# Kernel optimization log

Hardware: AMD Instinct MI355X
Metric: run time of the kernel (lower is better)

Reference implementation:

```python
import jax, jax.numpy as jnp
import numpy as np

D_MODEL = 2048
D_KV = 512
D_Q = 1536
N_HEADS = 16
HEAD_DIM = 128
ROPE_BASE = 10000.0


def apply_rope(x, past_len=0):
    # x: [B, H, S, D]; interleaved-pair rotation (pairs (2i, 2i+1))
    B, H, S, D = x.shape
    half = D // 2
    pos = (jnp.arange(S) + past_len).astype(jnp.float32)
    inv_freq = 1.0 / (ROPE_BASE ** (jnp.arange(half, dtype=jnp.float32) * 2.0 / D))
    ang = pos[:, None] * inv_freq[None, :]          # [S, half]
    cos, sin = jnp.cos(ang), jnp.sin(ang)
    x1 = x[..., 0::2]
    x2 = x[..., 1::2]
    r1 = x1 * cos - x2 * sin
    r2 = x1 * sin + x2 * cos
    return jnp.stack([r1, r2], axis=-1).reshape(x.shape)


def setup_inputs() -> dict:
    key = jax.random.key(0)
    ks = jax.random.split(key, 16)
    s = 0.02
    inp = {
        "h": jax.random.normal(ks[0], (2, 2048, D_MODEL), dtype=jnp.float32),
        # weights stored [in, out] (y = x @ W + b)
        "W_DKV": jax.random.normal(ks[1], (D_MODEL, D_KV)) * s,
        "b_DKV": jnp.zeros((D_KV,)),
        "W_UK": jax.random.normal(ks[2], (D_KV, N_HEADS * HEAD_DIM)) * s,
        "b_UK": jnp.zeros((N_HEADS * HEAD_DIM,)),
        "W_UV": jax.random.normal(ks[3], (D_KV, N_HEADS * HEAD_DIM)) * s,
        "b_UV": jnp.zeros((N_HEADS * HEAD_DIM,)),
        "W_DQ": jax.random.normal(ks[4], (D_MODEL, D_Q)) * s,
        "b_DQ": jnp.zeros((D_Q,)),
        "W_UQ": jax.random.normal(ks[5], (D_Q, N_HEADS * HEAD_DIM)) * s,
        "b_UQ": jnp.zeros((N_HEADS * HEAD_DIM,)),
        "W_KR": jax.random.normal(ks[6], (D_MODEL, D_MODEL)) * s,
        "b_KR": jnp.zeros((D_MODEL,)),
        "W_O": jax.random.normal(ks[7], (D_MODEL, D_MODEL)) * s,
        "b_O": jnp.zeros((D_MODEL,)),
    }
    return inp


def reference(h, W_DKV, b_DKV, W_UK, b_UK, W_UV, b_UV, W_DQ, b_DQ,
              W_UQ, b_UQ, W_KR, b_KR, W_O, b_O):
    B, S, _ = h.shape

    def split_heads(x):  # [B,S,H*D] -> [B,H,S,D]
        return x.reshape(B, S, N_HEADS, HEAD_DIM).transpose(0, 2, 1, 3)

    # latent KV path (prefill: no cache)
    c_KV = h @ W_DKV + b_DKV                     # [B,S,d_kv] latent cache
    k_C = split_heads(c_KV @ W_UK + b_UK)        # [B,H,S,Dh]
    v_C = split_heads(c_KV @ W_UV + b_UV)        # [B,H,S,Dh]

    # decoupled RoPE K path
    kr_cache = h @ W_KR + b_KR                   # [B,S,d_model]
    k_R = apply_rope(split_heads(kr_cache))      # [B,H,S,Dh]
    k = jnp.concatenate([k_C, k_R], axis=-1)     # [B,H,S,2*Dh]

    # latent Q path
    c_Q = h @ W_DQ + b_DQ
    q_C = split_heads(c_Q @ W_UQ + b_UQ)
    q_R = apply_rope(q_C, past_len=0)
    q = jnp.concatenate([q_C, q_R], axis=-1)     # [B,H,S,2*Dh]

    # causal attention
    scale = 1.0 / jnp.sqrt(jnp.float32(q.shape[-1]))
    scores = jnp.einsum("bhqd,bhkd->bhqk", q, k) * scale
    causal = jnp.tril(jnp.ones((S, S), dtype=bool))
    scores = jnp.where(causal, scores, jnp.finfo(scores.dtype).min)
    attn = jax.nn.softmax(scores, axis=-1)
    ctx = jnp.einsum("bhqk,bhkd->bhqd", attn, v_C)
    ctx = ctx.transpose(0, 2, 1, 3).reshape(B, S, N_HEADS * HEAD_DIM)
    out = ctx @ W_O + b_O
    return (out, c_KV, kr_cache)
```

## Files before the change

### kernel.cpp

```cpp
#include <hip/hip_runtime.h>
#include <cstdint>
#include <cstddef>

typedef __bf16 bf16;
typedef __bf16 bf16x8 __attribute__((ext_vector_type(8)));
typedef float  f32x4  __attribute__((ext_vector_type(4)));

#define INVF_C 0.20762050593046014f

__device__ __forceinline__ void async_copy16(const void* g, void* l)
{
    auto gp = (__attribute__((address_space(1))) const void*)(reinterpret_cast<uintptr_t>(g));
    auto lp = (__attribute__((address_space(3))) void*)(uint32_t)(reinterpret_cast<uintptr_t>(l));
    __builtin_amdgcn_global_load_lds(gp, lp, 16, 0, 0);
}

__global__ void cast_to_bf16(const float* __restrict__ in, bf16* __restrict__ out, int n)
{
    const int i = (blockIdx.x * 256 + threadIdx.x) * 4;
    if (i < n) {
        const float4 v = *(const float4*)(in + i);
        out[i]     = (bf16)v.x;
        out[i + 1] = (bf16)v.y;
        out[i + 2] = (bf16)v.z;
        out[i + 3] = (bf16)v.w;
    }
}

__global__ void transpose_cast(const float* __restrict__ in, bf16* __restrict__ out,
                               int R, int Ccols)
{
    __shared__ float tile[32][33];
    const int c0 = blockIdx.x * 32;
    const int r0 = blockIdx.y * 32;
    const int tx = threadIdx.x, ty = threadIdx.y;
    for (int i = ty; i < 32; i += 8)
        tile[i][tx] = in[(size_t)(r0 + i) * Ccols + c0 + tx];
    __syncthreads();
    for (int i = ty; i < 32; i += 8)
        out[(size_t)(c0 + i) * R + r0 + tx] = (bf16)tile[tx][i];
}

__device__ __forceinline__ void gemm_core(const bf16* __restrict__ A,
                                          const bf16* __restrict__ Bt,
                                          int K, int m0, int n0,
                                          bf16* As, bf16* Bs,
                                          f32x4 (&acc)[4][4])
{
    const int tid  = threadIdx.x;
    const int wave = tid >> 6;
    const int lane = tid & 63;
    const int quad = lane >> 4;
    const int l15  = lane & 15;
    const int wm   = (wave >> 1) * 64;
    const int wn   = (wave & 1) * 64;

    const int srow = lane >> 3;
    const int scol = (lane & 7) * 8;
    const bf16* Ab = A  + (size_t)(m0 + wave * 32 + srow) * K + scol;
    const bf16* Bb = Bt + (size_t)(n0 + wave * 32 + srow) * K + scol;
    bf16* AsW = &As[(wave * 32) * 64];
    bf16* BsW = &Bs[(wave * 32) * 64];

    for (int k0 = 0; k0 < K; k0 += 64) {
        __syncthreads();
#pragma unroll
        for (int i = 0; i < 4; ++i) {
            async_copy16(Ab + (size_t)(i * 8) * K + k0, AsW + i * 8 * 64);
            async_copy16(Bb + (size_t)(i * 8) * K + k0, BsW + i * 8 * 64);
        }
        __syncthreads();
#pragma unroll
        for (int ks = 0; ks < 2; ++ks) {
            bf16x8 af[4], bfr[4];
#pragma unroll
            for (int i = 0; i < 4; ++i)
                af[i] = *(const bf16x8*)&As[(wm + i * 16 + l15) * 64 + ks * 32 + quad * 8];
#pragma unroll
            for (int j = 0; j < 4; ++j)
                bfr[j] = *(const bf16x8*)&Bs[(wn + j * 16 + l15) * 64 + ks * 32 + quad * 8];
#pragma unroll
            for (int i = 0; i < 4; ++i)
#pragma unroll
                for (int j = 0; j < 4; ++j)
                    acc[i][j] = __builtin_amdgcn_mfma_f32_16x16x32_bf16(af[i], bfr[j], acc[i][j], 0, 0, 0);
        }
    }
}

__global__ __launch_bounds__(256, 2)
void gemm_bt(const bf16* __restrict__ A, const bf16* __restrict__ Bt,
             const float* __restrict__ bias, float* __restrict__ C,
             bf16* __restrict__ Cb, int M, int N, int K)
{
    __shared__ bf16 As[128 * 64];
    __shared__ bf16 Bs[128 * 64];
    const int m0 = blockIdx.y * 128;
    const int n0 = blockIdx.x * 128;
    f32x4 acc[4][4] = {};
    gemm_core(A, Bt, K, m0, n0, As, Bs, acc);

    const int tid  = threadIdx.x;
    const int wave = tid >> 6;
    const int lane = tid & 63;
    const int quad = lane >> 4;
    const int l15  = lane & 15;
    const int wm   = (wave >> 1) * 64;
    const int wn   = (wave & 1) * 64;

#pragma unroll
    for (int j = 0; j < 4; ++j) {
        const int col = n0 + wn + j * 16 + l15;
        const float bv = bias[col];
#pragma unroll
        for (int i = 0; i < 4; ++i) {
            const int row = m0 + wm + i * 16 + quad * 4;
#pragma unroll
            for (int r = 0; r < 4; ++r) {
                const float v = acc[i][j][r] + bv;
                if (C)  C [(size_t)(row + r) * N + col] = v;
                if (Cb) Cb[(size_t)(row + r) * N + col] = (bf16)v;
            }
        }
    }
}

__global__ __launch_bounds__(256, 2)
void gemm_batch1(const bf16* __restrict__ A, const bf16* __restrict__ WtAll,
                 const float* __restrict__ bDKV, const float* __restrict__ bKR,
                 const float* __restrict__ bDQ,
                 float* __restrict__ cKV_f, bf16* __restrict__ cKVb,
                 float* __restrict__ krc_f, bf16* __restrict__ cQ)
{
    __shared__ bf16 As[128 * 64];
    __shared__ bf16 Bs[128 * 64];
    const int m0 = blockIdx.y * 128;
    const int n0 = blockIdx.x * 128;
    f32x4 acc[4][4] = {};
    gemm_core(A, WtAll, 2048, m0, n0, As, Bs, acc);

    const int tid  = threadIdx.x;
    const int wave = tid >> 6;
    const int lane = tid & 63;
    const int quad = lane >> 4;
    const int l15  = lane & 15;
    const int wm   = (wave >> 1) * 64;
    const int wn   = (wave & 1) * 64;

    if (n0 < 512) {
#pragma unroll
        for (int j = 0; j < 4; ++j) {
            const int col = n0 + wn + j * 16 + l15;
            const float bv = bDKV[col];
#pragma unroll
            for (int i = 0; i < 4; ++i) {
                const int row = m0 + wm + i * 16 + quad * 4;
#pragma unroll
                for (int r = 0; r < 4; ++r) {
                    const float v = acc[i][j][r] + bv;
                    cKV_f[(size_t)(row + r) * 512 + col] = v;
                    cKVb [(size_t)(row + r) * 512 + col] = (bf16)v;
                }
            }
        }
    } else if (n0 < 2560) {
#pragma unroll
        for (int j = 0; j < 4; ++j) {
            const int col = n0 + wn + j * 16 + l15;
            const int cl  = col - 512;
            const float bv = bKR[cl];
#pragma unroll
            for (int i = 0; i < 4; ++i) {
                const int row = m0 + wm + i * 16 + quad * 4;
#pragma unroll
                for (int r = 0; r < 4; ++r)
                    krc_f[(size_t)(row + r) * 2048 + cl] = acc[i][j][r] + bv;
            }
        }
    } else {
#pragma unroll
        for (int j = 0; j < 4; ++j) {
            const int col = n0 + wn + j * 16 + l15;
            const int cl  = col - 2560;
            const float bv = bDQ[cl];
#pragma unroll
            for (int i = 0; i < 4; ++i) {
                const int row = m0 + wm + i * 16 + quad * 4;
#pragma unroll
                for (int r = 0; r < 4; ++r)
                    cQ[(size_t)(row + r) * 1536 + cl] = (bf16)(acc[i][j][r] + bv);
            }
        }
    }
}

__global__ __launch_bounds__(256, 2)
void gemm_batch45(const bf16* __restrict__ A, const bf16* __restrict__ Wt45,
                  const float* __restrict__ bUK, const float* __restrict__ bUV,
                  bf16* __restrict__ kC, bf16* __restrict__ vC)
{
    __shared__ bf16 As[128 * 64];
    __shared__ bf16 Bs[128 * 64];
    const int m0 = blockIdx.y * 128;
    const int n0 = blockIdx.x * 128;
    f32x4 acc[4][4] = {};
    gemm_core(A, Wt45, 512, m0, n0, As, Bs, acc);

    const int tid  = threadIdx.x;
    const int wave = tid >> 6;
    const int lane = tid & 63;
    const int quad = lane >> 4;
    const int l15  = lane & 15;
    const int wm   = (wave >> 1) * 64;
    const int wn   = (wave & 1) * 64;

    const bool isK = (n0 < 2048);
    bf16* outp = isK ? kC : vC;
    const float* bp = isK ? bUK : bUV;
    const int base = isK ? 0 : 2048;
#pragma unroll
    for (int j = 0; j < 4; ++j) {
        const int col = n0 + wn + j * 16 + l15;
        const int cl  = col - base;
        const float bv = bp[cl];
#pragma unroll
        for (int i = 0; i < 4; ++i) {
            const int row = m0 + wm + i * 16 + quad * 4;
#pragma unroll
            for (int r = 0; r < 4; ++r)
                outp[(size_t)(row + r) * 2048 + cl] = (bf16)(acc[i][j][r] + bv);
        }
    }
}

__global__ __launch_bounds__(256, 2)
void gemm_q_rope(const bf16* __restrict__ A, const bf16* __restrict__ Bt,
                 const float* __restrict__ bias,
                 bf16* __restrict__ qC, bf16* __restrict__ qR)
{
    __shared__ bf16 As[128 * 64];
    __shared__ bf16 Bs[128 * 64];
    const int m0 = blockIdx.y * 128;
    const int n0 = blockIdx.x * 128;
    f32x4 acc[4][4] = {};
    gemm_core(A, Bt, 1536, m0, n0, As, Bs, acc);

    const int tid  = threadIdx.x;
    const int wave = tid >> 6;
    const int lane = tid & 63;
    const int quad = lane >> 4;
    const int l15  = lane & 15;
    const int wm   = (wave >> 1) * 64;
    const int wn   = (wave & 1) * 64;
    const int odd  = l15 & 1;

#pragma unroll
    for (int j = 0; j < 4; ++j) {
        const int col = n0 + wn + j * 16 + l15;
        const float bv = bias[col];
        const float freq = exp2f(-(float)((col & 127) >> 1) * INVF_C);
#pragma unroll
        for (int i = 0; i < 4; ++i) {
            const int rowb = m0 + wm + i * 16 + quad * 4;
#pragma unroll
            for (int r = 0; r < 4; ++r) {
                const int row = rowb + r;
                const float v = acc[i][j][r] + bv;
                qC[(size_t)row * 2048 + col] = (bf16)v;
                const float vp = __shfl_xor(v, 1, 64);
                const float x1 = odd ? vp : v;
                const float x2 = odd ? v  : vp;
                const float ang = (float)(row & 2047) * freq;
                float sn, cs;
                __sincosf(ang, &sn, &cs);
                qR[(size_t)row * 2048 + col] =
                    (bf16)(odd ? (x1 * sn + x2 * cs) : (x1 * cs - x2 * sn));
            }
        }
    }
}

__global__ void transpose_v(const bf16* __restrict__ vC, bf16* __restrict__ vT)
{
    __shared__ bf16 tile[32][33];
    const int bh = blockIdx.z, b = bh >> 4, h = bh & 15;
    const int s0 = blockIdx.x * 32, d0 = blockIdx.y * 32;
    const int tx = threadIdx.x, ty = threadIdx.y;
    for (int i = ty; i < 32; i += 8)
        tile[i][tx] = vC[((size_t)(b * 2048 + s0 + i)) * 2048 + h * 128 + d0 + tx];
    __syncthreads();
    for (int i = ty; i < 32; i += 8)
        vT[((size_t)(bh * 128 + d0 + i)) * 2048 + s0 + tx] = tile[tx][i];
}

__global__ void rope_heads_f(const float* __restrict__ in, bf16* __restrict__ out)
{
    const int idx = blockIdx.x * 256 + threadIdx.x;
    const int j = idx & 63;
    const int h = (idx >> 6) & 15;
    const int s = (idx >> 10) & 2047;
    const int b = idx >> 21;
    const size_t src = ((size_t)(b * 2048 + s)) * 2048 + h * 128 + 2 * j;
    const float x1 = in[src], x2 = in[src + 1];
    const float ang = (float)s * exp2f(-(float)j * INVF_C);
    float sn, cs;
    __sincosf(ang, &sn, &cs);
    out[src]     = (bf16)(x1 * cs - x2 * sn);
    out[src + 1] = (bf16)(x1 * sn + x2 * cs);
}

__global__ __launch_bounds__(512, 2)
void mla_attn(const bf16* __restrict__ qCp, const bf16* __restrict__ qRp,
              const bf16* __restrict__ kCp, const bf16* __restrict__ kRp,
              const bf16* __restrict__ Vt, bf16* __restrict__ ctx)
{
    __shared__ bf16 Ks[64 * 264];
    __shared__ bf16 Vs[128 * 72];
    __shared__ bf16 Ps[128 * 72];
    const int bh   = blockIdx.x;
    const int b    = bh >> 4, hh = bh & 15;
    const int yq   = blockIdx.y;
    const int qt   = (yq < 8) ? (2 * yq) : (31 - 2 * yq);
    const int q0   = qt * 128;
    const int tid  = threadIdx.x;
    const int wave = tid >> 6;
    const int lane = tid & 63;
    const int quad = lane >> 4;
    const int l15  = lane & 15;
    const int wq   = q0 + wave * 16;

    bf16x8 qf[8];
    {
        const size_t qoff = ((size_t)(b * 2048 + wq + l15)) * 2048
                          + hh * 128 + quad * 8;
#pragma unroll
        for (int ks = 0; ks < 4; ++ks) {
            qf[ks]     = *(const bf16x8*)(qCp + qoff + ks * 32);
            qf[4 + ks] = *(const bf16x8*)(qRp + qoff + ks * 32);
        }
    }

    float mstate[4], lstate[4];
    f32x4 o[8];
#pragma unroll
    for (int r = 0; r < 4; ++r) { mstate[r] = -1e30f; lstate[r] = 0.0f; }
#pragma unroll
    for (int dt = 0; dt < 8; ++dt) { f32x4 z = {0.f, 0.f, 0.f, 0.f}; o[dt] = z; }

    const int krow = tid >> 4, kcol = (tid & 15) * 8;
    const int vsr  = tid >> 3, vsc  = (tid & 7) * 8;

    const int ntiles = 2 * qt + 2;
    for (int t = 0; t < ntiles; ++t) {
        const int kk0 = t * 64;
        __syncthreads();
#pragma unroll
        for (int it = 0; it < 2; ++it) {
            const int row = it * 32 + krow;
            const size_t g = ((size_t)(b * 2048 + kk0 + row)) * 2048 + hh * 128 + kcol;
            *(bf16x8*)&Ks[row * 264 + kcol]       = *(const bf16x8*)(kCp + g);
            *(bf16x8*)&Ks[row * 264 + 128 + kcol] = *(const bf16x8*)(kRp + g);
        }
#pragma unroll
        for (int it = 0; it < 2; ++it) {
            const int d = it * 64 + vsr;
            *(bf16x8*)&Vs[d * 72 + vsc] =
                *(const bf16x8*)(Vt + ((size_t)(bh * 128 + d)) * 2048 + kk0 + vsc);
        }
        __syncthreads();

        if (kk0 <= wq + 15) {
            f32x4 sc[4] = {};
#pragma unroll
            for (int ks = 0; ks < 8; ++ks)
#pragma unroll
                for (int j = 0; j < 4; ++j) {
                    bf16x8 kf = *(const bf16x8*)&Ks[(j * 16 + l15) * 264 + ks * 32 + quad * 8];
                    sc[j] = __builtin_amdgcn_mfma_f32_16x16x32_bf16(qf[ks], kf, sc[j], 0, 0, 0);
                }

            const bool diag = (kk0 + 63 > wq);
            float rowmax[4] = {-1e30f, -1e30f, -1e30f, -1e30f};
#pragma unroll
            for (int j = 0; j < 4; ++j) {
                const int kkcol = kk0 + j * 16 + l15;
#pragma unroll
                for (int r = 0; r < 4; ++r) {
                    float s = sc[j][r] * 0.0625f;
                    if (diag && (kkcol > wq + quad * 4 + r)) s = -1e30f;
                    sc[j][r] = s;
                    rowmax[r] = fmaxf(rowmax[r], s);
                }
            }
#pragma unroll
            for (int r = 0; r < 4; ++r) {
                float v = rowmax[r];
                v = fmaxf(v, __shfl_xor(v, 1, 64));
                v = fmaxf(v, __shfl_xor(v, 2, 64));
                v = fmaxf(v, __shfl_xor(v, 4, 64));
                v = fmaxf(v, __shfl_xor(v, 8, 64));
                rowmax[r] = v;
            }
            float alpha[4];
#pragma unroll
            for (int r = 0; r < 4; ++r) {
                const float mnew = fmaxf(mstate[r], rowmax[r]);
                alpha[r] = __expf(mstate[r] - mnew);
                mstate[r] = mnew;
            }
            float rowsum[4] = {0.f, 0.f, 0.f, 0.f};
#pragma unroll
            for (int j = 0; j < 4; ++j)
#pragma unroll
                for (int r = 0; r < 4; ++r) {
                    const float p = __expf(sc[j][r] - mstate[r]);
                    sc[j][r] = p;
                    rowsum[r] += p;
                }
#pragma unroll
            for (int r = 0; r < 4; ++r) {
                float v = rowsum[r];
                v += __shfl_xor(v, 1, 64);
                v += __shfl_xor(v, 2, 64);
                v += __shfl_xor(v, 4, 64);
                v += __shfl_xor(v, 8, 64);
                lstate[r] = lstate[r] * alpha[r] + v;
            }
#pragma unroll
            for (int j = 0; j < 4; ++j)
#pragma unroll
                for (int r = 0; r < 4; ++r)
                    Ps[(wave * 16 + quad * 4 + r) * 72 + j * 16 + l15] = (bf16)sc[j][r];
#pragma unroll
            for (int dt = 0; dt < 8; ++dt)
#pragma unroll
                for (int r = 0; r < 4; ++r)
                    o[dt][r] *= alpha[r];
#pragma unroll
            for (int ks2 = 0; ks2 < 2; ++ks2) {
                bf16x8 pf = *(const bf16x8*)&Ps[(wave * 16 + l15) * 72 + ks2 * 32 + quad * 8];
#pragma unroll
                for (int dt = 0; dt < 8; ++dt) {
                    bf16x8 vf = *(const bf16x8*)&Vs[(dt * 16 + l15) * 72 + ks2 * 32 + quad * 8];
                    o[dt] = __builtin_amdgcn_mfma_f32_16x16x32_bf16(pf, vf, o[dt], 0, 0, 0);
                }
            }
        }
    }

    float inv_l[4];
#pragma unroll
    for (int r = 0; r < 4; ++r) inv_l[r] = 1.0f / lstate[r];
#pragma unroll
    for (int dt = 0; dt < 8; ++dt) {
        const int d = dt * 16 + l15;
#pragma unroll
        for (int r = 0; r < 4; ++r) {
            const int q = wq + quad * 4 + r;
            ctx[((size_t)(b * 2048 + q)) * 2048 + hh * 128 + d] = (bf16)(o[dt][r] * inv_l[r]);
        }
    }
}

extern "C" void kernel_launch(void* const* d_in, const int* in_sizes, int n_in,
                              void* d_out, int out_size, void* d_ws, size_t ws_size,
                              hipStream_t stream)
{
    const float* h     = (const float*)d_in[0];
    const float* W_DKV = (const float*)d_in[1];
    const float* b_DKV = (const float*)d_in[2];
    const float* W_UK  = (const float*)d_in[3];
    const float* b_UK  = (const float*)d_in[4];
    const float* W_UV  = (const float*)d_in[5];
    const float* b_UV  = (const float*)d_in[6];
    const float* W_DQ  = (const float*)d_in[7];
    const float* b_DQ  = (const float*)d_in[8];
    const float* W_UQ  = (const float*)d_in[9];
    const float* b_UQ  = (const float*)d_in[10];
    const float* W_KR  = (const float*)d_in[11];
    const float* b_KR  = (const float*)d_in[12];
    const float* W_O   = (const float*)d_in[13];
    const float* b_O   = (const float*)d_in[14];

    float* out   = (float*)d_out;
    float* cKV_f = out + (size_t)8388608;
    float* krc_f = out + (size_t)10485760;

    bf16* qC = (bf16*)d_out;
    bf16* qR = (bf16*)d_out + 8388608;

    bf16* ws    = (bf16*)d_ws;
    bf16* hb    = ws + 0;
    bf16* cKVb  = ws + 8388608;
    bf16* cQ    = ws + 10485760;
    bf16* WtAll = ws + 16777216;
    bf16* kC    = ws + 25165824;
    bf16* vC    = ws + 33554432;
    bf16* kR    = hb;
    bf16* vT    = WtAll;
    bf16* ctx   = vC;

    dim3 tb(32, 8);

    cast_to_bf16<<<8192, 256, 0, stream>>>(h, hb, 8388608);

    transpose_cast<<<dim3(16, 64), tb, 0, stream>>>(W_DKV, WtAll,                 2048, 512);
    transpose_cast<<<dim3(64, 64), tb, 0, stream>>>(W_KR,  WtAll + 1048576,       2048, 2048);
    transpose_cast<<<dim3(48, 64), tb, 0, stream>>>(W_DQ,  WtAll + 5242880,       2048, 1536);

    gemm_batch1<<<dim3(32, 32), 256, 0, stream>>>(hb, WtAll, b_DKV, b_KR, b_DQ,
                                                  cKV_f, cKVb, krc_f, cQ);
    rope_heads_f<<<16384, 256, 0, stream>>>(krc_f, kR);

    transpose_cast<<<dim3(64, 16), tb, 0, stream>>>(W_UK, WtAll,           512, 2048);
    transpose_cast<<<dim3(64, 16), tb, 0, stream>>>(W_UV, WtAll + 1048576, 512, 2048);
    gemm_batch45<<<dim3(32, 32), 256, 0, stream>>>(cKVb, WtAll, b_UK, b_UV, kC, vC);

    transpose_cast<<<dim3(64, 48), tb, 0, stream>>>(W_UQ, WtAll, 1536, 2048);
    gemm_q_rope<<<dim3(16, 32), 256, 0, stream>>>(cQ, WtAll, b_UQ, qC, qR);

    transpose_v<<<dim3(64, 4, 32), tb, 0, stream>>>(vC, vT);

    mla_attn<<<dim3(32, 16), 512, 0, stream>>>(qC, qR, kC, kR, vT, ctx);

    transpose_cast<<<dim3(64, 64), tb, 0, stream>>>(W_O, WtAll, 2048, 2048);
    gemm_bt<<<dim3(16, 32), 256, 0, stream>>>(ctx, WtAll, b_O, out, nullptr, 4096, 2048, 2048);
}
```

Measured before the change: 541.1 us.

## Widen transpose tiles, swizzle GEMM blocks per XCD, lazy softmax rescale

The weight transpose-cast kernel now works on 64x64 tiles with float4 loads and paired bf16 stores, to cut memory-transaction overhead. All GEMM kernels remap block indices so consecutive tiles land on the same XCD, aiming for better L2 reuse. In the attention kernel, the online-softmax rescale of the output and running sum now happens only when some row max grows by more than a threshold. MFMA sections are bracketed with s_setprio raises. The lazy rescale gives up exact running-max tracking, which changes numerics slightly and relies on exp values staying bounded by the threshold.

New measurement: 591.3 us. 9.3% more time.

```diff
diff --git a/kernel.cpp b/kernel.cpp
--- a/kernel.cpp
+++ b/kernel.cpp
@@ -3,6 +3,7 @@
 #include <cstddef>
 
 typedef __bf16 bf16;
+typedef __bf16 bf16x2 __attribute__((ext_vector_type(2)));
 typedef __bf16 bf16x8 __attribute__((ext_vector_type(8)));
 typedef float  f32x4  __attribute__((ext_vector_type(4)));
 
@@ -27,18 +28,43 @@
     }
 }
 
-__global__ void transpose_cast(const float* __restrict__ in, bf16* __restrict__ out,
-                               int R, int Ccols)
-{
-    __shared__ float tile[32][33];
-    const int c0 = blockIdx.x * 32;
-    const int r0 = blockIdx.y * 32;
-    const int tx = threadIdx.x, ty = threadIdx.y;
-    for (int i = ty; i < 32; i += 8)
-        tile[i][tx] = in[(size_t)(r0 + i) * Ccols + c0 + tx];
+__global__ __launch_bounds__(256)
+void transpose_cast(const float* __restrict__ in, bf16* __restrict__ out,
+                    int R, int Ccols)
+{
+    __shared__ float tile[64][65];
+    const int c0 = blockIdx.x * 64;
+    const int r0 = blockIdx.y * 64;
+    const int tid = threadIdx.x;
+    const int lr = tid >> 4;
+    const int lc = (tid & 15) * 4;
+#pragma unroll
+    for (int i = 0; i < 4; ++i) {
+        const int row = i * 16 + lr;
+        const float4 v = *(const float4*)(in + (size_t)(r0 + row) * Ccols + c0 + lc);
+        tile[row][lc]     = v.x;
+        tile[row][lc + 1] = v.y;
+        tile[row][lc + 2] = v.z;
+        tile[row][lc + 3] = v.w;
+    }
     __syncthreads();
-    for (int i = ty; i < 32; i += 8)
-        out[(size_t)(c0 + i) * R + r0 + tx] = (bf16)tile[tx][i];
+    const int rr  = (tid & 31) * 2;
+    const int cc0 = tid >> 5;
+#pragma unroll
+    for (int i = 0; i < 8; ++i) {
+        const int cc = i * 8 + cc0;
+        bf16x2 p = { (bf16)tile[rr][cc], (bf16)tile[rr + 1][cc] };
+        *(bf16x2*)(out + (size_t)(c0 + cc) * R + r0 + rr) = p;
+    }
+}
+
+__device__ __forceinline__ void xcd_tile(int& m0, int& n0)
+{
+    const int bid = blockIdx.y * gridDim.x + blockIdx.x;
+    const int cpx = (gridDim.x * gridDim.y) >> 3;
+    const int swz = (bid & 7) * cpx + (bid >> 3);
+    m0 = (swz / gridDim.x) * 128;
+    n0 = (swz % gridDim.x) * 128;
 }
 
 __device__ __forceinline__ void gemm_core(const bf16* __restrict__ A,
@@ -95,8 +121,8 @@
 {
     __shared__ bf16 As[128 * 64];
     __shared__ bf16 Bs[128 * 64];
-    const int m0 = blockIdx.y * 128;
-    const int n0 = blockIdx.x * 128;
+    int m0, n0;
+    xcd_tile(m0, n0);
     f32x4 acc[4][4] = {};
     gemm_core(A, Bt, K, m0, n0, As, Bs, acc);
 
@@ -134,8 +160,8 @@
 {
     __shared__ bf16 As[128 * 64];
     __shared__ bf16 Bs[128 * 64];
-    const int m0 = blockIdx.y * 128;
-    const int n0 = blockIdx.x * 128;
+    int m0, n0;
+    xcd_tile(m0, n0);
     f32x4 acc[4][4] = {};
     gemm_core(A, WtAll, 2048, m0, n0, As, Bs, acc);
 
@@ -201,8 +227,8 @@
 {
     __shared__ bf16 As[128 * 64];
     __shared__ bf16 Bs[128 * 64];
-    const int m0 = blockIdx.y * 128;
-    const int n0 = blockIdx.x * 128;
+    int m0, n0;
+    xcd_tile(m0, n0);
     f32x4 acc[4][4] = {};
     gemm_core(A, Wt45, 512, m0, n0, As, Bs, acc);
 
@@ -240,8 +266,8 @@
 {
     __shared__ bf16 As[128 * 64];
     __shared__ bf16 Bs[128 * 64];
-    const int m0 = blockIdx.y * 128;
-    const int n0 = blockIdx.x * 128;
+    int m0, n0;
+    xcd_tile(m0, n0);
     f32x4 acc[4][4] = {};
     gemm_core(A, Bt, 1536, m0, n0, As, Bs, acc);
 
@@ -371,6 +397,7 @@
 
         if (kk0 <= wq + 15) {
             f32x4 sc[4] = {};
+            __builtin_amdgcn_s_setprio(1);
 #pragma unroll
             for (int ks = 0; ks < 8; ++ks)
 #pragma unroll
@@ -378,6 +405,7 @@
                     bf16x8 kf = *(const bf16x8*)&Ks[(j * 16 + l15) * 264 + ks * 32 + quad * 8];
                     sc[j] = __builtin_amdgcn_mfma_f32_16x16x32_bf16(qf[ks], kf, sc[j], 0, 0, 0);
                 }
+            __builtin_amdgcn_s_setprio(0);
 
             const bool diag = (kk0 + 63 > wq);
             float rowmax[4] = {-1e30f, -1e30f, -1e30f, -1e30f};
@@ -401,12 +429,24 @@
                 v = fmaxf(v, __shfl_xor(v, 8, 64));
                 rowmax[r] = v;
             }
-            float alpha[4];
-#pragma unroll
-            for (int r = 0; r < 4; ++r) {
-                const float mnew = fmaxf(mstate[r], rowmax[r]);
-                alpha[r] = __expf(mstate[r] - mnew);
-                mstate[r] = mnew;
+            const bool resc = __any((rowmax[0] > mstate[0] + 8.0f) |
+                                    (rowmax[1] > mstate[1] + 8.0f) |
+                                    (rowmax[2] > mstate[2] + 8.0f) |
+                                    (rowmax[3] > mstate[3] + 8.0f));
+            if (resc) {
+                float alpha[4];
+#pragma unroll
+                for (int r = 0; r < 4; ++r) {
+                    const float mnew = fmaxf(mstate[r], rowmax[r]);
+                    alpha[r] = __expf(mstate[r] - mnew);
+                    mstate[r] = mnew;
+                    lstate[r] *= alpha[r];
+                }
+#pragma unroll
+                for (int dt = 0; dt < 8; ++dt)
+#pragma unroll
+                    for (int r = 0; r < 4; ++r)
+                        o[dt][r] *= alpha[r];
             }
             float rowsum[4] = {0.f, 0.f, 0.f, 0.f};
 #pragma unroll
@@ -424,18 +464,14 @@
                 v += __shfl_xor(v, 2, 64);
                 v += __shfl_xor(v, 4, 64);
                 v += __shfl_xor(v, 8, 64);
-                lstate[r] = lstate[r] * alpha[r] + v;
+                lstate[r] += v;
             }
 #pragma unroll
             for (int j = 0; j < 4; ++j)
 #pragma unroll
                 for (int r = 0; r < 4; ++r)
                     Ps[(wave * 16 + quad * 4 + r) * 72 + j * 16 + l15] = (bf16)sc[j][r];
-#pragma unroll
-            for (int dt = 0; dt < 8; ++dt)
-#pragma unroll
-                for (int r = 0; r < 4; ++r)
-                    o[dt][r] *= alpha[r];
+            __builtin_amdgcn_s_setprio(1);
 #pragma unroll
             for (int ks2 = 0; ks2 < 2; ++ks2) {
                 bf16x8 pf = *(const bf16x8*)&Ps[(wave * 16 + l15) * 72 + ks2 * 32 + quad * 8];
@@ -445,6 +481,7 @@
                     o[dt] = __builtin_amdgcn_mfma_f32_16x16x32_bf16(pf, vf, o[dt], 0, 0, 0);
                 }
             }
+            __builtin_amdgcn_s_setprio(0);
         }
     }
 
@@ -504,25 +541,25 @@
 
     cast_to_bf16<<<8192, 256, 0, stream>>>(h, hb, 8388608);
 
-    transpose_cast<<<dim3(16, 64), tb, 0, stream>>>(W_DKV, WtAll,                 2048, 512);
-    transpose_cast<<<dim3(64, 64), tb, 0, stream>>>(W_KR,  WtAll + 1048576,       2048, 2048);
-    transpose_cast<<<dim3(48, 64), tb, 0, stream>>>(W_DQ,  WtAll + 5242880,       2048, 1536);
+    transpose_cast<<<dim3(8, 32),  256, 0, stream>>>(W_DKV, WtAll,           2048, 512);
+    transpose_cast<<<dim3(32, 32), 256, 0, stream>>>(W_KR,  WtAll + 1048576, 2048, 2048);
+    transpose_cast<<<dim3(24, 32), 256, 0, stream>>>(W_DQ,  WtAll + 5242880, 2048, 1536);
 
     gemm_batch1<<<dim3(32, 32), 256, 0, stream>>>(hb, WtAll, b_DKV, b_KR, b_DQ,
                                                   cKV_f, cKVb, krc_f, cQ);
     rope_heads_f<<<16384, 256, 0, stream>>>(krc_f, kR);
 
-    transpose_cast<<<dim3(64, 16), tb, 0, stream>>>(W_UK, WtAll,           512, 2048);
-    transpose_cast<<<dim3(64, 16), tb, 0, stream>>>(W_UV, WtAll + 1048576, 512, 2048);
+    transpose_cast<<<dim3(32, 8), 256, 0, stream>>>(W_UK, WtAll,           512, 2048);
+    transpose_cast<<<dim3(32, 8), 256, 0, stream>>>(W_UV, WtAll + 1048576, 512, 2048);
     gemm_batch45<<<dim3(32, 32), 256, 0, stream>>>(cKVb, WtAll, b_UK, b_UV, kC, vC);
 
-    transpose_cast<<<dim3(64, 48), tb, 0, stream>>>(W_UQ, WtAll, 1536, 2048);
+    transpose_cast<<<dim3(32, 24), 256, 0, stream>>>(W_UQ, WtAll, 1536, 2048);
     gemm_q_rope<<<dim3(16, 32), 256, 0, stream>>>(cQ, WtAll, b_UQ, qC, qR);
 
     transpose_v<<<dim3(64, 4, 32), tb, 0, stream>>>(vC, vT);
 
     mla_attn<<<dim3(32, 16), 512, 0, stream>>>(qC, qR, kC, kR, vT, ctx);
 
-    transpose_cast<<<dim3(64, 64), tb, 0, stream>>>(W_O, WtAll, 2048, 2048);
+    transpose_cast<<<dim3(32, 32), 256, 0, stream>>>(W_O, WtAll, 2048, 2048);
     gemm_bt<<<dim3(16, 32), 256, 0, stream>>>(ctx, WtAll, b_O, out, nullptr, 4096, 2048, 2048);
 }
```
